# Kernel optimization log

Measured on AMD Instinct MI355X. Metric: run time of the kernel, lower is better.

## Reference

```python
import jax, jax.numpy as jnp
import numpy as np

N_FRUSTUMS = 14400  # n_splits_azi(360) * n_splits_pol(40)
N_POINTS = 2_000_000
N_CHANNELS = 8


def setup_inputs() -> dict:
    key = jax.random.key(0)
    k1, k2 = jax.random.split(key)
    pc = jax.random.normal(k1, (N_POINTS, N_CHANNELS), dtype=jnp.float32)
    i_frustum = jnp.sort(
        jax.random.randint(k2, (N_POINTS,), 0, N_FRUSTUMS)
    ).astype(jnp.int32)
    i_inv = jnp.arange(N_POINTS, dtype=jnp.int32)  # identity inverse permutation
    counts_padded = jnp.bincount(i_frustum, length=N_FRUSTUMS).astype(jnp.float32)
    return {
        "pc": pc,
        "i_frustum": i_frustum,
        "i_inv": i_inv,
        "counts_padded": counts_padded,
    }


def reference(pc, i_frustum, i_inv, counts_padded):
    """Faithful port of symmetrize_mean / symmetrize_std / symmetrize_max plus the
    gather-broadcast normalize (pc - mean[i_frustum][i_inv]) / std.

    pc:            [N, C] float point features
    i_frustum:     [N]   int point->frustum segment ids (sorted)
    i_inv:         [N]   int inverse permutation applied after gather
    counts_padded: [F]   float per-frustum point counts (0 for empty frustums)
    """
    n_frustums = counts_padded.shape[0]
    nonempty = counts_padded[:, None] != 0.0  # [F, 1]
    safe_counts = jnp.maximum(counts_padded, 1.0)[:, None]  # avoid div-by-zero

    # symmetrize_mean: scatter_add then divide where count != 0
    sums = jax.ops.segment_sum(pc, i_frustum, num_segments=n_frustums)  # [F, C]
    mean = jnp.where(nonempty, sums / safe_counts, sums)

    # symmetrize_std: scatter_add of squared deviation, divide, sqrt where > 0
    dev = pc - mean[i_frustum][i_inv]  # [N, C] gather-broadcast subtract
    var_sums = jax.ops.segment_sum(dev * dev, i_frustum, num_segments=n_frustums)
    var = jnp.where(nonempty, var_sums / safe_counts, var_sums)
    std = jnp.where(var > 0.0, jnp.sqrt(jnp.maximum(var, 0.0)), var)

    # symmetrize_max: scatter_reduce amax onto a zeros-initialized buffer
    # (include_self=True default in torch => result is max(0, segment max))
    frustum_max = jnp.zeros((n_frustums, pc.shape[1]), pc.dtype).at[i_frustum].max(pc)

    # gather-broadcast normalize (decorator_distance_to_mean style, with per-frustum std)
    std_g = std[i_frustum][i_inv]
    pc_norm = dev / jnp.where(std_g > 0.0, std_g, 1.0)

    return mean, std, frustum_max, pc_norm
```

## Files before the change

### kernel.cpp

```cpp
#include <hip/hip_runtime.h>

#define NCH 8
#define CACHE 8

typedef float v4f __attribute__((ext_vector_type(4)));

__device__ __forceinline__ v4f norm4(const float4& v, const float4& m, const float4& d) {
    v4f o;
    o.x = (v.x - m.x) * d.x;
    o.y = (v.y - m.y) * d.y;
    o.z = (v.z - m.z) * d.z;
    o.w = (v.w - m.w) * d.w;
    return o;
}

__device__ __forceinline__ int wave_lower_bound(const int* __restrict__ a, int n, int key,
                                                int lane) {
    int lo = 0, len = n;
    while (len > 64) {
        int step = (len + 63) >> 6;
        int p = lo + lane * step;
        int v = (p < lo + len) ? a[p] : 0x7fffffff;
        unsigned long long bal = __ballot(v < key);
        int cnt = __popcll(bal);
        if (cnt == 0) return lo;
        int nlo = lo + (cnt - 1) * step + 1;
        int nhi = lo + len;
        int cap = lo + cnt * step;
        if (cnt < 64 && cap < nhi) nhi = cap;
        lo = nlo; len = nhi - nlo;
    }
    int v = (lane < len) ? a[lo + lane] : 0x7fffffff;
    unsigned long long bal = __ballot(v < key);
    return lo + __popcll(bal);
}

__global__ __launch_bounds__(128) void k_fused(
    const float* __restrict__ pc, const int* __restrict__ i_frustum,
    const float* __restrict__ counts, int n, int F,
    float* __restrict__ out_mean, float* __restrict__ out_std,
    float* __restrict__ out_max, float* __restrict__ out_pcn)
{
    const int wid = (blockIdx.x * blockDim.x + threadIdx.x) >> 6;
    if (wid >= F) return;
    const int lane = threadIdx.x & 63;

    const int s = wave_lower_bound(i_frustum, n, wid, lane);
    const float cnt = counts[wid];
    const int e = s + (int)cnt;

    const float4* __restrict__ pc4 = reinterpret_cast<const float4*>(pc);
    v4f* __restrict__ out4 = reinterpret_cast<v4f*>(out_pcn);

    const int b = s * 2, E = e * 2;
    const int lim = max(E - 1, 0);

    float4 sum = {0.f, 0.f, 0.f, 0.f};
    float4 sq  = {0.f, 0.f, 0.f, 0.f};
    float4 mx  = {0.f, 0.f, 0.f, 0.f};
    float4 c[CACHE];

    {
        int k = b + lane;
        #pragma unroll
        for (int u = 0; u < CACHE; ++u) {
            c[u] = pc4[min(k, lim)];
            k += 64;
        }
    }
    {
        int k = b + lane;
        #pragma unroll
        for (int u = 0; u < CACHE; ++u) {
            const bool in = k < E;
            float vx = in ? c[u].x : 0.f, vy = in ? c[u].y : 0.f;
            float vz = in ? c[u].z : 0.f, vw = in ? c[u].w : 0.f;
            sum.x += vx; sq.x += vx * vx; mx.x = fmaxf(mx.x, vx);
            sum.y += vy; sq.y += vy * vy; mx.y = fmaxf(mx.y, vy);
            sum.z += vz; sq.z += vz * vz; mx.z = fmaxf(mx.z, vz);
            sum.w += vw; sq.w += vw * vw; mx.w = fmaxf(mx.w, vw);
            k += 64;
        }
        for (int kk = b + lane + CACHE * 64; kk < E; kk += 64) {
            float4 v = pc4[kk];
            sum.x += v.x; sq.x += v.x * v.x; mx.x = fmaxf(mx.x, v.x);
            sum.y += v.y; sq.y += v.y * v.y; mx.y = fmaxf(mx.y, v.y);
            sum.z += v.z; sq.z += v.z * v.z; mx.z = fmaxf(mx.z, v.z);
            sum.w += v.w; sq.w += v.w * v.w; mx.w = fmaxf(mx.w, v.w);
        }
    }

    #pragma unroll
    for (int m = 2; m <= 32; m <<= 1) {
        sum.x += __shfl_xor(sum.x, m, 64);
        sum.y += __shfl_xor(sum.y, m, 64);
        sum.z += __shfl_xor(sum.z, m, 64);
        sum.w += __shfl_xor(sum.w, m, 64);
        sq.x  += __shfl_xor(sq.x,  m, 64);
        sq.y  += __shfl_xor(sq.y,  m, 64);
        sq.z  += __shfl_xor(sq.z,  m, 64);
        sq.w  += __shfl_xor(sq.w,  m, 64);
        mx.x = fmaxf(mx.x, __shfl_xor(mx.x, m, 64));
        mx.y = fmaxf(mx.y, __shfl_xor(mx.y, m, 64));
        mx.z = fmaxf(mx.z, __shfl_xor(mx.z, m, 64));
        mx.w = fmaxf(mx.w, __shfl_xor(mx.w, m, 64));
    }

    const float invc = 1.0f / fmaxf(cnt, 1.0f);
    float4 mean, sd, dv;
    mean.x = sum.x * invc; mean.y = sum.y * invc; mean.z = sum.z * invc; mean.w = sum.w * invc;
    float vx = fmaxf(sq.x * invc - mean.x * mean.x, 0.0f);
    float vy = fmaxf(sq.y * invc - mean.y * mean.y, 0.0f);
    float vz = fmaxf(sq.z * invc - mean.z * mean.z, 0.0f);
    float vw = fmaxf(sq.w * invc - mean.w * mean.w, 0.0f);
    sd.x = sqrtf(vx); sd.y = sqrtf(vy); sd.z = sqrtf(vz); sd.w = sqrtf(vw);
    dv.x = 1.0f / (sd.x > 0.f ? sd.x : 1.f);
    dv.y = 1.0f / (sd.y > 0.f ? sd.y : 1.f);
    dv.z = 1.0f / (sd.z > 0.f ? sd.z : 1.f);
    dv.w = 1.0f / (sd.w > 0.f ? sd.w : 1.f);

    if (lane < 2) {
        reinterpret_cast<float4*>(out_mean + (size_t)wid * NCH)[lane] = mean;
        reinterpret_cast<float4*>(out_std  + (size_t)wid * NCH)[lane] = sd;
        reinterpret_cast<float4*>(out_max  + (size_t)wid * NCH)[lane] = mx;
    }

    {
        int k = b + lane;
        #pragma unroll
        for (int u = 0; u < CACHE; ++u) {
            if (k < E) {
                v4f o = norm4(c[u], mean, dv);
                __builtin_nontemporal_store(o, &out4[k]);
            }
            k += 64;
        }
        for (int kk = b + lane + CACHE * 64; kk < E; kk += 64) {
            v4f o = norm4(pc4[kk], mean, dv);
            __builtin_nontemporal_store(o, &out4[kk]);
        }
    }
}

extern "C" void kernel_launch(void* const* d_in, const int* in_sizes, int n_in,
                              void* d_out, int out_size, void* d_ws, size_t ws_size,
                              hipStream_t stream) {
    const float* pc        = (const float*)d_in[0];
    const int*   i_frustum = (const int*)d_in[1];
    const float* counts    = (const float*)d_in[3];

    int n = in_sizes[0] / NCH;
    int F = in_sizes[3];

    float* out_mean = (float*)d_out;
    float* out_std  = out_mean + (size_t)F * NCH;
    float* out_max  = out_std  + (size_t)F * NCH;
    float* out_pcn  = out_max  + (size_t)F * NCH;

    int waves_per_block = 128 / 64;
    int blocks = (F + waves_per_block - 1) / waves_per_block;
    k_fused<<<blocks, 128, 0, stream>>>(pc, i_frustum, counts, n, F,
                                        out_mean, out_std, out_max, out_pcn);
}
```

Baseline: 30.13 us.

## Split fused stats/normalize kernel into separate stats and point-parallel normalize kernels

Splits the single per-frustum kernel into two. The first computes mean, std and max per frustum. The second is a flat point-parallel kernel that gathers each point's mean and std by frustum id and writes the normalized output. This removes the wave-per-frustum load imbalance on the write path and improves parallelism for the store phase. In exchange it launches a second kernel, re-reads pc from memory instead of from registers, and adds an i_frustum gather plus per-element divides.

After: 47.15 us. 56.5% more time.

```diff
diff --git a/kernel.cpp b/kernel.cpp
--- a/kernel.cpp
+++ b/kernel.cpp
@@ -4,15 +4,6 @@
 #define CACHE 8
 
 typedef float v4f __attribute__((ext_vector_type(4)));
-
-__device__ __forceinline__ v4f norm4(const float4& v, const float4& m, const float4& d) {
-    v4f o;
-    o.x = (v.x - m.x) * d.x;
-    o.y = (v.y - m.y) * d.y;
-    o.z = (v.z - m.z) * d.z;
-    o.w = (v.w - m.w) * d.w;
-    return o;
-}
 
 __device__ __forceinline__ int wave_lower_bound(const int* __restrict__ a, int n, int key,
                                                 int lane) {
@@ -35,11 +26,11 @@
     return lo + __popcll(bal);
 }
 
-__global__ __launch_bounds__(128) void k_fused(
+__global__ __launch_bounds__(128) void k_stats2(
     const float* __restrict__ pc, const int* __restrict__ i_frustum,
     const float* __restrict__ counts, int n, int F,
     float* __restrict__ out_mean, float* __restrict__ out_std,
-    float* __restrict__ out_max, float* __restrict__ out_pcn)
+    float* __restrict__ out_max)
 {
     const int wid = (blockIdx.x * blockDim.x + threadIdx.x) >> 6;
     if (wid >= F) return;
@@ -50,8 +41,6 @@
     const int e = s + (int)cnt;
 
     const float4* __restrict__ pc4 = reinterpret_cast<const float4*>(pc);
-    v4f* __restrict__ out4 = reinterpret_cast<v4f*>(out_pcn);
-
     const int b = s * 2, E = e * 2;
     const int lim = max(E - 1, 0);
 
@@ -106,40 +95,42 @@
         mx.w = fmaxf(mx.w, __shfl_xor(mx.w, m, 64));
     }
 
-    const float invc = 1.0f / fmaxf(cnt, 1.0f);
-    float4 mean, sd, dv;
-    mean.x = sum.x * invc; mean.y = sum.y * invc; mean.z = sum.z * invc; mean.w = sum.w * invc;
-    float vx = fmaxf(sq.x * invc - mean.x * mean.x, 0.0f);
-    float vy = fmaxf(sq.y * invc - mean.y * mean.y, 0.0f);
-    float vz = fmaxf(sq.z * invc - mean.z * mean.z, 0.0f);
-    float vw = fmaxf(sq.w * invc - mean.w * mean.w, 0.0f);
-    sd.x = sqrtf(vx); sd.y = sqrtf(vy); sd.z = sqrtf(vz); sd.w = sqrtf(vw);
-    dv.x = 1.0f / (sd.x > 0.f ? sd.x : 1.f);
-    dv.y = 1.0f / (sd.y > 0.f ? sd.y : 1.f);
-    dv.z = 1.0f / (sd.z > 0.f ? sd.z : 1.f);
-    dv.w = 1.0f / (sd.w > 0.f ? sd.w : 1.f);
-
     if (lane < 2) {
+        const float invc = 1.0f / fmaxf(cnt, 1.0f);
+        float4 mean, sd;
+        mean.x = sum.x * invc; mean.y = sum.y * invc;
+        mean.z = sum.z * invc; mean.w = sum.w * invc;
+        float vx = fmaxf(sq.x * invc - mean.x * mean.x, 0.0f);
+        float vy = fmaxf(sq.y * invc - mean.y * mean.y, 0.0f);
+        float vz = fmaxf(sq.z * invc - mean.z * mean.z, 0.0f);
+        float vw = fmaxf(sq.w * invc - mean.w * mean.w, 0.0f);
+        sd.x = sqrtf(vx); sd.y = sqrtf(vy); sd.z = sqrtf(vz); sd.w = sqrtf(vw);
         reinterpret_cast<float4*>(out_mean + (size_t)wid * NCH)[lane] = mean;
         reinterpret_cast<float4*>(out_std  + (size_t)wid * NCH)[lane] = sd;
         reinterpret_cast<float4*>(out_max  + (size_t)wid * NCH)[lane] = mx;
     }
+}
 
-    {
-        int k = b + lane;
-        #pragma unroll
-        for (int u = 0; u < CACHE; ++u) {
-            if (k < E) {
-                v4f o = norm4(c[u], mean, dv);
-                __builtin_nontemporal_store(o, &out4[k]);
-            }
-            k += 64;
-        }
-        for (int kk = b + lane + CACHE * 64; kk < E; kk += 64) {
-            v4f o = norm4(pc4[kk], mean, dv);
-            __builtin_nontemporal_store(o, &out4[kk]);
-        }
-    }
+__global__ __launch_bounds__(256) void k_norm2(
+    const float* __restrict__ pc, const int* __restrict__ i_frustum,
+    const float* __restrict__ meanb, const float* __restrict__ stdb,
+    float* __restrict__ out_pcn, int n4)
+{
+    const int t = blockIdx.x * blockDim.x + threadIdx.x;
+    if (t >= n4) return;
+    const int i = t >> 1, half = t & 1;
+    const int f = i_frustum[i];
+
+    const float4 m = reinterpret_cast<const float4*>(meanb + (size_t)f * NCH)[half];
+    const float4 sd = reinterpret_cast<const float4*>(stdb + (size_t)f * NCH)[half];
+    const float4 p = reinterpret_cast<const float4*>(pc)[t];
+
+    v4f o;
+    o.x = (p.x - m.x) / (sd.x > 0.f ? sd.x : 1.f);
+    o.y = (p.y - m.y) / (sd.y > 0.f ? sd.y : 1.f);
+    o.z = (p.z - m.z) / (sd.z > 0.f ? sd.z : 1.f);
+    o.w = (p.w - m.w) / (sd.w > 0.f ? sd.w : 1.f);
+    __builtin_nontemporal_store(o, &reinterpret_cast<v4f*>(out_pcn)[t]);
 }
 
 extern "C" void kernel_launch(void* const* d_in, const int* in_sizes, int n_in,
@@ -159,6 +150,10 @@
 
     int waves_per_block = 128 / 64;
     int blocks = (F + waves_per_block - 1) / waves_per_block;
-    k_fused<<<blocks, 128, 0, stream>>>(pc, i_frustum, counts, n, F,
-                                        out_mean, out_std, out_max, out_pcn);
+    k_stats2<<<blocks, 128, 0, stream>>>(pc, i_frustum, counts, n, F,
+                                         out_mean, out_std, out_max);
+
+    int n4 = n * 2;
+    int nblocks = (n4 + 255) / 256;
+    k_norm2<<<nblocks, 256, 0, stream>>>(pc, i_frustum, out_mean, out_std, out_pcn, n4);
 }
```
